# Performance work log

Hardware: AMD Instinct MI355X
Metric: run time of the kernel (lower is better)

The kernel has to match this reference:

```python
import jax, jax.numpy as jnp
import numpy as np

EPS = 1e-8

def setup_inputs() -> dict:
    key = jax.random.key(0)
    k1, k2 = jax.random.split(key)
    B, D, H, W, K = 32, 256, 64, 64, 64
    X = jax.random.normal(k1, (B, D, H, W), dtype=jnp.float32)
    std1 = 1.0 / float(np.sqrt(K * D))
    codewords = jax.random.uniform(k2, (K, D), dtype=jnp.float32, minval=-std1, maxval=std1)
    return {"X": X, "codewords": codewords}

def reference(X, codewords):
    B, D = X.shape[0], X.shape[1]
    # (B, D, H, W) -> (B, N, D)
    Xf = X.reshape(B, D, -1).transpose(0, 2, 1)
    # pairwise cosine similarity: normalize then matmul -> (B, N, K)
    Xn = Xf / jnp.maximum(jnp.linalg.norm(Xf, axis=-1, keepdims=True), EPS)
    Cn = codewords / jnp.maximum(jnp.linalg.norm(codewords, axis=-1, keepdims=True), EPS)
    L = jnp.einsum('bnd,kd->bnk', Xn, Cn)
    A = jax.nn.softmax(L, axis=2)
    # aggregate: E[b,k,d] = sum_n A[b,n,k] * (Xf[b,n,d] - C[k,d])
    # expressed without materializing the (B,N,K,D) residual tensor:
    E = jnp.einsum('bnk,bnd->bkd', A, Xf) - A.sum(axis=1)[:, :, None] * codewords[None, :, :]
    return E
```

## Files before the change

### kernel.cpp

```cpp
#include <hip/hip_runtime.h>
#include <hip/hip_bf16.h>
#include <math.h>

#define BB 32
#define DD 256
#define NN 4096
#define KK 64
#define EPSV 1e-8f
#define XSTR 264

typedef __attribute__((ext_vector_type(8))) short short8;
typedef __attribute__((ext_vector_type(4))) float f32x4;

__device__ __forceinline__ unsigned int bf16pair(float a, float b) {
    __hip_bfloat162 h = __float22bfloat162_rn(make_float2(a, b));
    return *(unsigned int*)&h;
}
__device__ __forceinline__ unsigned short bf16one(float a) {
    unsigned int ua = __float_as_uint(a);
    ua += 0x7fffu + ((ua >> 16) & 1u);
    return (unsigned short)(ua >> 16);
}

__device__ __forceinline__ void stage_group(int dbase, int n4, const float4* rr,
                                            unsigned short* xnd_s, unsigned short* xdn_s,
                                            f32x4& ssn) {
    float4 r0 = rr[0], r1 = rr[1], r2 = rr[2], r3 = rr[3];
    ssn.x = fmaf(r0.x, r0.x, ssn.x); ssn.x = fmaf(r1.x, r1.x, ssn.x);
    ssn.x = fmaf(r2.x, r2.x, ssn.x); ssn.x = fmaf(r3.x, r3.x, ssn.x);
    ssn.y = fmaf(r0.y, r0.y, ssn.y); ssn.y = fmaf(r1.y, r1.y, ssn.y);
    ssn.y = fmaf(r2.y, r2.y, ssn.y); ssn.y = fmaf(r3.y, r3.y, ssn.y);
    ssn.z = fmaf(r0.z, r0.z, ssn.z); ssn.z = fmaf(r1.z, r1.z, ssn.z);
    ssn.z = fmaf(r2.z, r2.z, ssn.z); ssn.z = fmaf(r3.z, r3.z, ssn.z);
    ssn.w = fmaf(r0.w, r0.w, ssn.w); ssn.w = fmaf(r1.w, r1.w, ssn.w);
    ssn.w = fmaf(r2.w, r2.w, ssn.w); ssn.w = fmaf(r3.w, r3.w, ssn.w);
#pragma unroll
    for (int j = 0; j < 4; j++) {
        int d = dbase + j;
        uint2 u;
        u.x = bf16pair(rr[j].x, rr[j].y);
        u.y = bf16pair(rr[j].z, rr[j].w);
        *(uint2*)(xdn_s + d * 64 + ((((n4 >> 3) ^ (d & 7)) << 3) | (n4 & 7))) = u;
    }
    {
        float col[4][4] = {{r0.x, r1.x, r2.x, r3.x},
                           {r0.y, r1.y, r2.y, r3.y},
                           {r0.z, r1.z, r2.z, r3.z},
                           {r0.w, r1.w, r2.w, r3.w}};
#pragma unroll
        for (int j = 0; j < 4; j++) {
            int n = n4 + j;
            uint2 u;
            u.x = bf16pair(col[j][0], col[j][1]);
            u.y = bf16pair(col[j][2], col[j][3]);
            int blk = (dbase >> 3) ^ ((n >> 2) & 3);
            *(uint2*)(xnd_s + n * XSTR + (blk << 3) + (dbase & 7)) = u;
        }
    }
}

__global__ __launch_bounds__(256, 2) void k_fused(const float* __restrict__ X,
                                                  const float* __restrict__ C,
                                                  float* __restrict__ P,
                                                  float* __restrict__ Sp) {
    __shared__ unsigned short xnd_s[64 * XSTR];
    __shared__ unsigned short xdn_s[DD * 64];
    __shared__ unsigned short at_s[KK * 72];
    __shared__ float rn4[4 * 64];
    __shared__ float red_s[4 * 64];

    int t = threadIdx.x;
    int b = blockIdx.x >> 4, chunk = blockIdx.x & 15;
    int w = t >> 6, lane = t & 63, c = lane & 15, g = lane >> 4;
    int q = t >> 4;
    int n4 = c * 4;

    const float* Xb = X + (size_t)b * DD * NN + chunk * 256;

    float4 pre[8];
#pragma unroll
    for (int i = 0; i < 2; i++) {
        const float* xb = Xb + (size_t)(q * 4 + 64 * i) * NN + n4;
#pragma unroll
        for (int j = 0; j < 4; j++) pre[i * 4 + j] = *(const float4*)(xb + (size_t)j * NN);
    }

    short8 cnf[8];
    {
        int k = 16 * w + c;
        const float* cp = C + k * DD;
        float4 v0[8], v1[8];
        float ss = 0.f;
#pragma unroll
        for (int ks = 0; ks < 8; ks++) {
            v0[ks] = *(const float4*)(cp + 32 * ks + 8 * g);
            v1[ks] = *(const float4*)(cp + 32 * ks + 8 * g + 4);
            ss = fmaf(v0[ks].x, v0[ks].x, ss); ss = fmaf(v0[ks].y, v0[ks].y, ss);
            ss = fmaf(v0[ks].z, v0[ks].z, ss); ss = fmaf(v0[ks].w, v0[ks].w, ss);
            ss = fmaf(v1[ks].x, v1[ks].x, ss); ss = fmaf(v1[ks].y, v1[ks].y, ss);
            ss = fmaf(v1[ks].z, v1[ks].z, ss); ss = fmaf(v1[ks].w, v1[ks].w, ss);
        }
        ss += __shfl_xor(ss, 16);
        ss += __shfl_xor(ss, 32);
        float r = 1.f / fmaxf(sqrtf(ss), EPSV);
#pragma unroll
        for (int ks = 0; ks < 8; ks++) {
            uint4 u;
            u.x = bf16pair(v0[ks].x * r, v0[ks].y * r);
            u.y = bf16pair(v0[ks].z * r, v0[ks].w * r);
            u.z = bf16pair(v1[ks].x * r, v1[ks].y * r);
            u.w = bf16pair(v1[ks].z * r, v1[ks].w * r);
            cnf[ks] = *(short8*)&u;
        }
    }

    f32x4 eacc[4][4];
#pragma unroll
    for (int dt = 0; dt < 4; dt++)
#pragma unroll
        for (int kt = 0; kt < 4; kt++) eacc[dt][kt] = (f32x4){0.f, 0.f, 0.f, 0.f};
    float s_acc[4] = {0.f, 0.f, 0.f, 0.f};

    for (int p = 0; p < 4; p++) {
        float4 cur[8];
#pragma unroll
        for (int i = 0; i < 2; i++) {
            const float* xb = Xb + (size_t)(q * 4 + 64 * (2 + i)) * NN + p * 64 + n4;
#pragma unroll
            for (int j = 0; j < 4; j++) cur[i * 4 + j] = *(const float4*)(xb + (size_t)j * NN);
        }
        __syncthreads();

        f32x4 ssn = (f32x4){0.f, 0.f, 0.f, 0.f};
#pragma unroll
        for (int i = 0; i < 2; i++)
            stage_group(q * 4 + 64 * i, n4, &pre[i * 4], xnd_s, xdn_s, ssn);
#pragma unroll
        for (int i = 0; i < 2; i++)
            stage_group(q * 4 + 64 * (2 + i), n4, &cur[i * 4], xnd_s, xdn_s, ssn);

        if (p < 3) {
#pragma unroll
            for (int i = 0; i < 2; i++) {
                const float* xb = Xb + (size_t)(q * 4 + 64 * i) * NN + (p + 1) * 64 + n4;
#pragma unroll
                for (int j = 0; j < 4; j++) pre[i * 4 + j] = *(const float4*)(xb + (size_t)j * NN);
            }
        }

        ssn.x += __shfl_xor(ssn.x, 16); ssn.x += __shfl_xor(ssn.x, 32);
        ssn.y += __shfl_xor(ssn.y, 16); ssn.y += __shfl_xor(ssn.y, 32);
        ssn.z += __shfl_xor(ssn.z, 16); ssn.z += __shfl_xor(ssn.z, 32);
        ssn.w += __shfl_xor(ssn.w, 16); ssn.w += __shfl_xor(ssn.w, 32);
        if (g == 0) *(f32x4*)(rn4 + w * 64 + n4) = ssn;

        __syncthreads();

        f32x4 lacc[4];
#pragma unroll
        for (int nt = 0; nt < 4; nt++) lacc[nt] = (f32x4){0.f, 0.f, 0.f, 0.f};
#pragma unroll
        for (int ks = 0; ks < 8; ks++) {
            short8 af = cnf[ks];
#pragma unroll
            for (int nt = 0; nt < 4; nt++) {
                int n = nt * 16 + c;
                short8 bf = *(const short8*)(xnd_s + n * XSTR +
                                             (((4 * ks + g) ^ ((n >> 2) & 3)) << 3));
                lacc[nt] = __builtin_amdgcn_mfma_f32_16x16x32_bf16(af, bf, lacc[nt], 0, 0, 0);
            }
        }

        float lv[4][4];
#pragma unroll
        for (int nt = 0; nt < 4; nt++) {
            int n = nt * 16 + c;
            float ssq = rn4[n] + rn4[64 + n] + rn4[128 + n] + rn4[192 + n];
            float rn = 1.f / fmaxf(sqrtf(ssq), EPSV);
            float s = 0.f;
#pragma unroll
            for (int r = 0; r < 4; r++) {
                lv[nt][r] = __expf(lacc[nt][r] * rn);
                s += lv[nt][r];
            }
            s += __shfl_xor(s, 16);
            s += __shfl_xor(s, 32);
            if (g == 0) red_s[w * 64 + n] = s;
        }
        __syncthreads();

#pragma unroll
        for (int nt = 0; nt < 4; nt++) {
            int n = nt * 16 + c;
            float denom = red_s[n] + red_s[64 + n] + red_s[128 + n] + red_s[192 + n];
            float inv = 1.f / denom;
#pragma unroll
            for (int r = 0; r < 4; r++) {
                float a = lv[nt][r] * inv;
                s_acc[r] += a;
                int k = 16 * w + 4 * g + r;
                at_s[k * 72 + ((((n >> 3) ^ (k & 7)) << 3) | (n & 7))] = bf16one(a);
            }
        }
        __syncthreads();

#pragma unroll
        for (int ks2 = 0; ks2 < 2; ks2++) {
            short8 bk[4];
#pragma unroll
            for (int kt = 0; kt < 4; kt++) {
                int k = kt * 16 + c;
                bk[kt] = *(const short8*)(at_s + k * 72 + (((4 * ks2 + g) ^ (k & 7)) << 3));
            }
#pragma unroll
            for (int dt = 0; dt < 4; dt++) {
                int d = w * 64 + dt * 16 + c;
                short8 af = *(const short8*)(xdn_s + d * 64 + (((4 * ks2 + g) ^ (d & 7)) << 3));
#pragma unroll
                for (int kt = 0; kt < 4; kt++)
                    eacc[dt][kt] =
                        __builtin_amdgcn_mfma_f32_16x16x32_bf16(af, bk[kt], eacc[dt][kt], 0, 0, 0);
            }
        }
    }

    float* Pb = P + (size_t)blockIdx.x * (DD * KK);
#pragma unroll
    for (int dt = 0; dt < 4; dt++)
#pragma unroll
        for (int kt = 0; kt < 4; kt++)
#pragma unroll
            for (int r = 0; r < 4; r++) {
                int d = w * 64 + dt * 16 + 4 * g + r;
                Pb[d * 64 + kt * 16 + c] = eacc[dt][kt][r];
            }
#pragma unroll
    for (int r = 0; r < 4; r++) {
        float v = s_acc[r];
        v += __shfl_xor(v, 1);
        v += __shfl_xor(v, 2);
        v += __shfl_xor(v, 4);
        v += __shfl_xor(v, 8);
        if (c == 0) Sp[blockIdx.x * 64 + 16 * w + 4 * g + r] = v;
    }
}

__global__ __launch_bounds__(256) void k_fin(const float* __restrict__ P,
                                             const float* __restrict__ Sp,
                                             const float* __restrict__ C,
                                             float* __restrict__ out) {
    int idx = blockIdx.x * 256 + threadIdx.x;
    int b = idx >> 14;
    int r = idx & 16383;
    int d = r >> 6;
    int k = r & 63;
    float e = 0.f, s = 0.f;
    int base = b * 16;
#pragma unroll
    for (int cc = 0; cc < 16; cc++) {
        e += P[(size_t)(base + cc) * (DD * KK) + d * 64 + k];
        s += Sp[(base + cc) * 64 + k];
    }
    out[(size_t)(b * 64 + k) * 256 + d] = e - s * C[k * 256 + d];
}

extern "C" void kernel_launch(void* const* d_in, const int* in_sizes, int n_in,
                              void* d_out, int out_size, void* d_ws, size_t ws_size,
                              hipStream_t stream) {
    const float* X = (const float*)d_in[0];
    const float* C = (const float*)d_in[1];
    float* out = (float*)d_out;
    unsigned char* ws = (unsigned char*)d_ws;

    float* Sp = (float*)ws;
    float* P = (float*)(ws + 131072);

    k_fused<<<512, 256, 0, stream>>>(X, C, P, Sp);
    k_fin<<<2048, 256, 0, stream>>>(P, Sp, C, out);
}
```

Before: 214.2 us.

## Precompute bf16 normalized codewords and transpose similarity MFMA to keep softmax in-wave

Adds a small prep kernel that normalizes the codewords and converts them to bf16 once, so the fused kernel reads codeword fragments from global/L2 instead of recomputing them per block. The similarity MFMA is swapped so each wave owns 16 pixels and all 64 codewords. The softmax denominator then becomes a shuffle reduction inside the wave, which removes one block-wide barrier and its shared-memory round trip. All four d-groups of X are now prefetched one step ahead into registers, raising register pressure. It also adds an extra kernel launch and global loads inside the inner loop.

```diff
diff --git a/kernel.cpp b/kernel.cpp
--- a/kernel.cpp
+++ b/kernel.cpp
@@ -20,6 +20,36 @@
     unsigned int ua = __float_as_uint(a);
     ua += 0x7fffu + ((ua >> 16) & 1u);
     return (unsigned short)(ua >> 16);
+}
+
+__global__ __launch_bounds__(256) void k_prep(const float* __restrict__ C,
+                                              unsigned short* __restrict__ Cnb) {
+    __shared__ float rcn_s[KK];
+    int t = threadIdx.x;
+    if (t < KK) {
+        const float4* c4 = (const float4*)(C + t * DD);
+        float ss = 0.f;
+#pragma unroll 8
+        for (int i = 0; i < DD / 4; i++) {
+            float4 v = c4[i];
+            ss = fmaf(v.x, v.x, ss);
+            ss = fmaf(v.y, v.y, ss);
+            ss = fmaf(v.z, v.z, ss);
+            ss = fmaf(v.w, v.w, ss);
+        }
+        rcn_s[t] = 1.f / fmaxf(sqrtf(ss), EPSV);
+    }
+    __syncthreads();
+    int k = t >> 2, d0 = (t & 3) * 64;
+    float r = rcn_s[k];
+#pragma unroll
+    for (int j = 0; j < 64; j += 4) {
+        float4 v = *(const float4*)(C + k * DD + d0 + j);
+        uint2 u;
+        u.x = bf16pair(v.x * r, v.y * r);
+        u.y = bf16pair(v.z * r, v.w * r);
+        *(uint2*)(Cnb + k * DD + d0 + j) = u;
+    }
 }
 
 __device__ __forceinline__ void stage_group(int dbase, int n4, const float4* rr,
@@ -60,58 +90,30 @@
 }
 
 __global__ __launch_bounds__(256, 2) void k_fused(const float* __restrict__ X,
-                                                  const float* __restrict__ C,
+                                                  const unsigned short* __restrict__ Cnb,
                                                   float* __restrict__ P,
                                                   float* __restrict__ Sp) {
     __shared__ unsigned short xnd_s[64 * XSTR];
     __shared__ unsigned short xdn_s[DD * 64];
     __shared__ unsigned short at_s[KK * 72];
     __shared__ float rn4[4 * 64];
-    __shared__ float red_s[4 * 64];
+    __shared__ float s_red[4 * 64];
 
     int t = threadIdx.x;
     int b = blockIdx.x >> 4, chunk = blockIdx.x & 15;
     int w = t >> 6, lane = t & 63, c = lane & 15, g = lane >> 4;
     int q = t >> 4;
     int n4 = c * 4;
+    int c7 = c & 7;
 
     const float* Xb = X + (size_t)b * DD * NN + chunk * 256;
 
-    float4 pre[8];
-#pragma unroll
-    for (int i = 0; i < 2; i++) {
+    float4 pre[16];
+#pragma unroll
+    for (int i = 0; i < 4; i++) {
         const float* xb = Xb + (size_t)(q * 4 + 64 * i) * NN + n4;
 #pragma unroll
         for (int j = 0; j < 4; j++) pre[i * 4 + j] = *(const float4*)(xb + (size_t)j * NN);
-    }
-
-    short8 cnf[8];
-    {
-        int k = 16 * w + c;
-        const float* cp = C + k * DD;
-        float4 v0[8], v1[8];
-        float ss = 0.f;
-#pragma unroll
-        for (int ks = 0; ks < 8; ks++) {
-            v0[ks] = *(const float4*)(cp + 32 * ks + 8 * g);
-            v1[ks] = *(const float4*)(cp + 32 * ks + 8 * g + 4);
-            ss = fmaf(v0[ks].x, v0[ks].x, ss); ss = fmaf(v0[ks].y, v0[ks].y, ss);
-            ss = fmaf(v0[ks].z, v0[ks].z, ss); ss = fmaf(v0[ks].w, v0[ks].w, ss);
-            ss = fmaf(v1[ks].x, v1[ks].x, ss); ss = fmaf(v1[ks].y, v1[ks].y, ss);
-            ss = fmaf(v1[ks].z, v1[ks].z, ss); ss = fmaf(v1[ks].w, v1[ks].w, ss);
-        }
-        ss += __shfl_xor(ss, 16);
-        ss += __shfl_xor(ss, 32);
-        float r = 1.f / fmaxf(sqrtf(ss), EPSV);
-#pragma unroll
-        for (int ks = 0; ks < 8; ks++) {
-            uint4 u;
-            u.x = bf16pair(v0[ks].x * r, v0[ks].y * r);
-            u.y = bf16pair(v0[ks].z * r, v0[ks].w * r);
-            u.z = bf16pair(v1[ks].x * r, v1[ks].y * r);
-            u.w = bf16pair(v1[ks].z * r, v1[ks].w * r);
-            cnf[ks] = *(short8*)&u;
-        }
     }
 
     f32x4 eacc[4][4];
@@ -122,26 +124,16 @@
     float s_acc[4] = {0.f, 0.f, 0.f, 0.f};
 
     for (int p = 0; p < 4; p++) {
-        float4 cur[8];
-#pragma unroll
-        for (int i = 0; i < 2; i++) {
-            const float* xb = Xb + (size_t)(q * 4 + 64 * (2 + i)) * NN + p * 64 + n4;
-#pragma unroll
-            for (int j = 0; j < 4; j++) cur[i * 4 + j] = *(const float4*)(xb + (size_t)j * NN);
-        }
         __syncthreads();
 
         f32x4 ssn = (f32x4){0.f, 0.f, 0.f, 0.f};
 #pragma unroll
-        for (int i = 0; i < 2; i++)
+        for (int i = 0; i < 4; i++)
             stage_group(q * 4 + 64 * i, n4, &pre[i * 4], xnd_s, xdn_s, ssn);
-#pragma unroll
-        for (int i = 0; i < 2; i++)
-            stage_group(q * 4 + 64 * (2 + i), n4, &cur[i * 4], xnd_s, xdn_s, ssn);
 
         if (p < 3) {
 #pragma unroll
-            for (int i = 0; i < 2; i++) {
+            for (int i = 0; i < 4; i++) {
                 const float* xb = Xb + (size_t)(q * 4 + 64 * i) * NN + (p + 1) * 64 + n4;
 #pragma unroll
                 for (int j = 0; j < 4; j++) pre[i * 4 + j] = *(const float4*)(xb + (size_t)j * NN);
@@ -158,47 +150,51 @@
 
         f32x4 lacc[4];
 #pragma unroll
-        for (int nt = 0; nt < 4; nt++) lacc[nt] = (f32x4){0.f, 0.f, 0.f, 0.f};
+        for (int kt = 0; kt < 4; kt++) lacc[kt] = (f32x4){0.f, 0.f, 0.f, 0.f};
+        const unsigned short* xr = xnd_s + (16 * w + c) * XSTR;
 #pragma unroll
         for (int ks = 0; ks < 8; ks++) {
-            short8 af = cnf[ks];
-#pragma unroll
-            for (int nt = 0; nt < 4; nt++) {
-                int n = nt * 16 + c;
-                short8 bf = *(const short8*)(xnd_s + n * XSTR +
-                                             (((4 * ks + g) ^ ((n >> 2) & 3)) << 3));
-                lacc[nt] = __builtin_amdgcn_mfma_f32_16x16x32_bf16(af, bf, lacc[nt], 0, 0, 0);
-            }
-        }
-
+            int kss = (ks + 2 * p) & 7;
+            short8 af = *(const short8*)(xr + (((4 * kss + g) ^ (c >> 2)) << 3));
+#pragma unroll
+            for (int kt = 0; kt < 4; kt++) {
+                short8 bf = *(const short8*)(Cnb + (16 * kt + c) * DD + 32 * kss + 8 * g);
+                lacc[kt] = __builtin_amdgcn_mfma_f32_16x16x32_bf16(af, bf, lacc[kt], 0, 0, 0);
+            }
+        }
+
+        float rnv[4];
+#pragma unroll
+        for (int r = 0; r < 4; r++) {
+            int n = 16 * w + 4 * g + r;
+            float ssq = rn4[n] + rn4[64 + n] + rn4[128 + n] + rn4[192 + n];
+            rnv[r] = 1.f / fmaxf(sqrtf(ssq), EPSV);
+        }
         float lv[4][4];
-#pragma unroll
-        for (int nt = 0; nt < 4; nt++) {
-            int n = nt * 16 + c;
-            float ssq = rn4[n] + rn4[64 + n] + rn4[128 + n] + rn4[192 + n];
-            float rn = 1.f / fmaxf(sqrtf(ssq), EPSV);
-            float s = 0.f;
+        float sden[4] = {0.f, 0.f, 0.f, 0.f};
+#pragma unroll
+        for (int kt = 0; kt < 4; kt++)
 #pragma unroll
             for (int r = 0; r < 4; r++) {
-                lv[nt][r] = __expf(lacc[nt][r] * rn);
-                s += lv[nt][r];
-            }
-            s += __shfl_xor(s, 16);
-            s += __shfl_xor(s, 32);
-            if (g == 0) red_s[w * 64 + n] = s;
-        }
-        __syncthreads();
-
-#pragma unroll
-        for (int nt = 0; nt < 4; nt++) {
-            int n = nt * 16 + c;
-            float denom = red_s[n] + red_s[64 + n] + red_s[128 + n] + red_s[192 + n];
-            float inv = 1.f / denom;
+                lv[kt][r] = __expf(lacc[kt][r] * rnv[r]);
+                sden[r] += lv[kt][r];
+            }
+#pragma unroll
+        for (int r = 0; r < 4; r++) {
+            sden[r] += __shfl_xor(sden[r], 1);
+            sden[r] += __shfl_xor(sden[r], 2);
+            sden[r] += __shfl_xor(sden[r], 4);
+            sden[r] += __shfl_xor(sden[r], 8);
+            sden[r] = 1.f / sden[r];
+        }
+#pragma unroll
+        for (int kt = 0; kt < 4; kt++) {
+            int k = 16 * kt + c;
 #pragma unroll
             for (int r = 0; r < 4; r++) {
-                float a = lv[nt][r] * inv;
-                s_acc[r] += a;
-                int k = 16 * w + 4 * g + r;
+                float a = lv[kt][r] * sden[r];
+                s_acc[kt] += a;
+                int n = 16 * w + 4 * g + r;
                 at_s[k * 72 + ((((n >> 3) ^ (k & 7)) << 3) | (n & 7))] = bf16one(a);
             }
         }
@@ -215,7 +211,7 @@
 #pragma unroll
             for (int dt = 0; dt < 4; dt++) {
                 int d = w * 64 + dt * 16 + c;
-                short8 af = *(const short8*)(xdn_s + d * 64 + (((4 * ks2 + g) ^ (d & 7)) << 3));
+                short8 af = *(const short8*)(xdn_s + d * 64 + (((4 * ks2 + g) ^ c7) << 3));
 #pragma unroll
                 for (int kt = 0; kt < 4; kt++)
                     eacc[dt][kt] =
@@ -235,14 +231,14 @@
                 Pb[d * 64 + kt * 16 + c] = eacc[dt][kt][r];
             }
 #pragma unroll
-    for (int r = 0; r < 4; r++) {
-        float v = s_acc[r];
-        v += __shfl_xor(v, 1);
-        v += __shfl_xor(v, 2);
-        v += __shfl_xor(v, 4);
-        v += __shfl_xor(v, 8);
-        if (c == 0) Sp[blockIdx.x * 64 + 16 * w + 4 * g + r] = v;
-    }
+    for (int kt = 0; kt < 4; kt++) {
+        float v = s_acc[kt];
+        v += __shfl_xor(v, 16);
+        v += __shfl_xor(v, 32);
+        if (g == 0) s_red[w * 64 + 16 * kt + c] = v;
+    }
+    __syncthreads();
+    if (t < 64) Sp[blockIdx.x * 64 + t] = s_red[t] + s_red[64 + t] + s_red[128 + t] + s_red[192 + t];
 }
 
 __global__ __launch_bounds__(256) void k_fin(const float* __restrict__ P,
@@ -272,9 +268,11 @@
     float* out = (float*)d_out;
     unsigned char* ws = (unsigned char*)d_ws;
 
-    float* Sp = (float*)ws;
-    float* P = (float*)(ws + 131072);
-
-    k_fused<<<512, 256, 0, stream>>>(X, C, P, Sp);
+    unsigned short* Cnb = (unsigned short*)ws;
+    float* Sp = (float*)(ws + 32768);
+    float* P = (float*)(ws + 32768 + 131072);
+
+    k_prep<<<1, 256, 0, stream>>>(C, Cnb);
+    k_fused<<<512, 256, 0, stream>>>(X, Cnb, P, Sp);
     k_fin<<<2048, 256, 0, stream>>>(P, Sp, C, out);
 }
```

Result: slower. 247.9 us (+15.7%).
